# Kernel tuning notes

Hardware: AMD Instinct MI355X
Metric: run time of the kernel (lower is better)

Reference implementation:

```python
import jax, jax.numpy as jnp
import numpy as np
import math

N_NODES = 100000
D = 64
N_EDGES = 1280000
LN_EPS = 1e-5


def setup_inputs() -> dict:
    key = jax.random.key(0)
    ks = jax.random.split(key, 8)
    x = jax.random.normal(ks[0], (N_NODES, D), dtype=jnp.float32)
    edge_index = jax.random.randint(ks[1], (2, N_EDGES), 0, N_NODES, dtype=jnp.int64)
    # xavier_uniform with gain=0.1 for weight matrices
    limit = 0.1 * math.sqrt(6.0 / (D + D))
    qk_w = jax.random.uniform(ks[2], (D, D), dtype=jnp.float32, minval=-limit, maxval=limit)
    v_w = jax.random.uniform(ks[3], (D, D), dtype=jnp.float32, minval=-limit, maxval=limit)
    o_w = jax.random.uniform(ks[4], (D, D), dtype=jnp.float32, minval=-limit, maxval=limit)
    qk_b = jnp.zeros((D,), dtype=jnp.float32)
    v_b = jnp.zeros((D,), dtype=jnp.float32)
    o_b = jnp.zeros((D,), dtype=jnp.float32)
    ln_g = jnp.ones((D,), dtype=jnp.float32)
    ln_b = jnp.zeros((D,), dtype=jnp.float32)
    return {"x": x, "edge_index": edge_index, "qk_w": qk_w, "qk_b": qk_b,
            "v_w": v_w, "v_b": v_b, "o_w": o_w, "o_b": o_b,
            "ln_g": ln_g, "ln_b": ln_b}


def reference(x, edge_index, qk_w, qk_b, v_w, v_b, o_w, o_b, ln_g, ln_b):
    n = x.shape[0]
    # shared Q/K projection and V projection (torch Linear: x @ W^T + b)
    qk = x @ qk_w.T + qk_b            # [N, D]
    v = x @ v_w.T + v_b               # [N, D]

    src = edge_index[0]
    dst = edge_index[1]

    # edge-wise attention logits: <q[dst], k[src]> / sqrt(D), clamped
    scores = jnp.sum(qk[dst] * qk[src], axis=-1) / math.sqrt(v.shape[-1])  # [E]
    scores = jnp.clip(scores, -5.0, 5.0)

    # segment softmax over incoming edges of each destination node
    seg_max = jax.ops.segment_max(scores, dst, num_segments=n)   # [N], -inf for empty
    e = jnp.exp(scores - seg_max[dst])                           # [E]
    seg_sum = jax.ops.segment_sum(e, dst, num_segments=n)        # [N]
    attn = e / seg_sum[dst]                                      # [E]

    # weighted scatter-add aggregation (nodes with no in-edges stay zero)
    out = jax.ops.segment_sum(attn[:, None] * v[src], dst, num_segments=n)  # [N, D]

    out = out @ o_w.T + o_b

    # LayerNorm(out + residual)
    h = out + x
    mu = jnp.mean(h, axis=-1, keepdims=True)
    var = jnp.mean(jnp.square(h - mu), axis=-1, keepdims=True)
    h = (h - mu) * jax.lax.rsqrt(var + LN_EPS)
    return h * ln_g + ln_b
```

## Files before the change

### kernel.cpp

```cpp
#include <hip/hip_runtime.h>
#include <hip/hip_bf16.h>
#include <math.h>

#define DD 64
#define CAP 64
#define BINSZ 256
#define SLOTS 16
#define EPB 1024
#define NBINS 391
#define LN_EPS 1e-5f

typedef float v2f __attribute__((ext_vector_type(2)));
typedef __attribute__((ext_vector_type(8))) short bf16x8;
typedef __attribute__((ext_vector_type(4))) float f32x4;

__device__ __forceinline__ float bf2f(unsigned short u) {
    return __uint_as_float(((unsigned)u) << 16);
}
__device__ __forceinline__ short f2bf(float f) {
    __hip_bfloat16 h = __float2bfloat16(f);
    return *reinterpret_cast<short*>(&h);
}
__device__ __forceinline__ bf16x8 cvt8(const float* p) {
    float4 a = *(const float4*)p;
    float4 b = *(const float4*)(p + 4);
    bf16x8 r;
    r[0] = f2bf(a.x); r[1] = f2bf(a.y); r[2] = f2bf(a.z); r[3] = f2bf(a.w);
    r[4] = f2bf(b.x); r[5] = f2bf(b.y); r[6] = f2bf(b.z); r[7] = f2bf(b.w);
    return r;
}
__device__ __forceinline__ unsigned char f2fp8(float f) {
    return (unsigned char)(__builtin_amdgcn_cvt_pk_fp8_f32(f, 0.f, 0, false) & 0xff);
}

__global__ __launch_bounds__(256) void prep_kernel(
    const float* __restrict__ x,
    const float* __restrict__ qk_w, const float* __restrict__ qk_b,
    const float* __restrict__ v_w,  const float* __restrict__ v_b,
    const int* __restrict__ eidx, int* __restrict__ cnttab,
    unsigned* __restrict__ ebuf,
    __hip_bfloat16* __restrict__ qk, unsigned char* __restrict__ kv,
    int n, int E, int AB)
{
    __shared__ int lhist[NBINS];
    __shared__ unsigned char lkv[64 * 128];
    __shared__ unsigned short lq[64 * 64];

    int bid = blockIdx.x;
    int tid = threadIdx.x;
    if (bid < AB) {
        for (int b = tid; b < NBINS; b += 256) lhist[b] = 0;
        __syncthreads();
        int nv = E >> 2;
        int i4 = bid * 256 + tid;
        unsigned* slab = ebuf + (size_t)bid * NBINS * SLOTS;
        if (i4 < nv) {
            uint4 d = ((const uint4*)(eidx + E))[i4];
            uint4 s = ((const uint4*)(eidx))[i4];
            #pragma unroll
            for (int c = 0; c < 4; ++c) {
                unsigned dd = (c == 0) ? d.x : (c == 1) ? d.y
                            : (c == 2) ? d.z : d.w;
                unsigned ss = (c == 0) ? s.x : (c == 1) ? s.y
                            : (c == 2) ? s.z : s.w;
                int bin = dd >> 8;
                int r = atomicAdd(&lhist[bin], 1);
                if (r < SLOTS)
                    slab[bin * SLOTS + r] = (ss << 8) | (dd & 255);
            }
        }
        __syncthreads();
        int* mycnt = cnttab + bid * NBINS;
        for (int b = tid; b < NBINS; b += 256)
            mycnt[b] = min(lhist[b], SLOTS);
    } else {
        int pbid = bid - AB;
        int wave = tid >> 6, lane = tid & 63;
        int node0 = pbid * 64 + wave * 16;
        int lr = lane & 15;
        int lk = (lane >> 4) << 3;

        if (node0 < n) {
            int arow = min(node0 + lr, n - 1);
            const float* xr = x + (size_t)arow * 64 + lk;
            bf16x8 A0 = cvt8(xr);
            bf16x8 A1 = cvt8(xr + 32);

            float qbias[4] = {qk_b[lr], qk_b[16 + lr], qk_b[32 + lr], qk_b[48 + lr]};
            float vbias[4] = {v_b[lr],  v_b[16 + lr],  v_b[32 + lr],  v_b[48 + lr]};

            f32x4 z = {0.f, 0.f, 0.f, 0.f};
            f32x4 accq[4], accv[4];
            #pragma unroll
            for (int ct = 0; ct < 4; ++ct) {
                const float* wq = qk_w + (size_t)(ct * 16 + lr) * 64 + lk;
                bf16x8 Bq0 = cvt8(wq);
                bf16x8 Bq1 = cvt8(wq + 32);
                f32x4 aq = __builtin_amdgcn_mfma_f32_16x16x32_bf16(A0, Bq0, z, 0, 0, 0);
                aq = __builtin_amdgcn_mfma_f32_16x16x32_bf16(A1, Bq1, aq, 0, 0, 0);
                accq[ct] = aq;
                const float* wv = v_w + (size_t)(ct * 16 + lr) * 64 + lk;
                bf16x8 Bv0 = cvt8(wv);
                bf16x8 Bv1 = cvt8(wv + 32);
                f32x4 av = __builtin_amdgcn_mfma_f32_16x16x32_bf16(A0, Bv0, z, 0, 0, 0);
                av = __builtin_amdgcn_mfma_f32_16x16x32_bf16(A1, Bv1, av, 0, 0, 0);
                accv[ct] = av;
            }
            #pragma unroll
            for (int ct = 0; ct < 4; ++ct) {
                int dim  = ct * 16 + lr;
                int koff = ((dim >> 2) << 3) + (dim & 3);
                #pragma unroll
                for (int r = 0; r < 4; ++r) {
                    int ndl = wave * 16 + ((lane >> 4) << 2) + r;
                    float q = accq[ct][r] + qbias[ct];
                    float v = accv[ct][r] + vbias[ct];
                    lq[ndl * 64 + dim] = (unsigned short)f2bf(q);
                    lkv[ndl * 128 + koff]     = f2fp8(q);
                    lkv[ndl * 128 + koff + 4] = f2fp8(v);
                }
            }
        }
        __syncthreads();
        int row = tid >> 2;
        size_t gnode = (size_t)pbid * 64 + row;
        if (gnode < (size_t)n) {
            const uint4* skv = (const uint4*)(lkv + tid * 32);
            uint4* dkv = (uint4*)(kv + (size_t)pbid * 64 * 128 + tid * 32);
            dkv[0] = skv[0];
            dkv[1] = skv[1];
            const uint4* sq = (const uint4*)((const unsigned char*)lq + tid * 32);
            uint4* dq = (uint4*)((unsigned char*)qk + (size_t)pbid * 64 * 128 + tid * 32);
            dq[0] = sq[0];
            dq[1] = sq[1];
        }
    }
}

__global__ __launch_bounds__(512) void bucket_kernel(
    const int* __restrict__ cnttab, const unsigned* __restrict__ ebuf,
    int* __restrict__ deg, int* __restrict__ bucket, int n, int NPB)
{
    __shared__ int lbkt[BINSZ * CAP];
    __shared__ int ldeg[BINSZ];
    int bin = blockIdx.x, tid = threadIdx.x;
    if (tid < BINSZ) ldeg[tid] = 0;
    __syncthreads();
    for (int c = tid; c < NPB; c += 512) {
        int cnt = cnttab[c * NBINS + bin];
        const unsigned* run = ebuf + ((size_t)c * NBINS + bin) * SLOTS;
        for (int r = 0; r < cnt; ++r) {
            unsigned e = run[r];
            int rel = e & 255;
            int rr = atomicAdd(&ldeg[rel], 1);
            if (rr < CAP) lbkt[(rel << 6) + rr] = (int)(e >> 8);
        }
    }
    __syncthreads();
    size_t gbase = (size_t)(bin << 8) << 6;
    int node0 = bin << 8;
    const uint4* src = (const uint4*)lbkt;
    uint4* dst = (uint4*)(bucket + gbase);
    for (int i = tid; i < BINSZ * CAP / 4; i += 512) {
        if (node0 + (i >> 4) < n) dst[i] = src[i];
    }
    if (tid < BINSZ) {
        int node = node0 + tid;
        if (node < n) deg[node] = min(ldeg[tid], CAP);
    }
}

__global__ __launch_bounds__(256) void attn_kernel(
    const __hip_bfloat16* __restrict__ qk, const unsigned char* __restrict__ kv,
    const int* __restrict__ deg, const int* __restrict__ bucket,
    __hip_bfloat16* __restrict__ outd, int n)
{
    int tid = threadIdx.x;
    int wave = tid >> 6, lane = tid & 63;
    int node = blockIdx.x * 4 + wave;
    if (node >= n) return;

    int sub = lane >> 4;
    int sl  = lane & 15;

    ushort4 qu = *(const ushort4*)(qk + ((size_t)node << 6) + (sl << 2));
    v2f qlo = {bf2f(qu.x), bf2f(qu.y)};
    v2f qhi = {bf2f(qu.z), bf2f(qu.w)};
    int dn = deg[node];
    int medge = bucket[((size_t)node << 6) + lane];

    float s = 0.f;
    v2f acclo = {0.f, 0.f};
    v2f acchi = {0.f, 0.f};
    const float ESCALE = 0.18033688f;

    for (int base = 0; base < dn; base += 16) {
        int m1 = dn - 1;
        int i0 = base + sub;
        int i1 = i0 + 4, i2 = i0 + 8, i3 = i0 + 12;
        int s0 = __shfl(medge, min(i0, m1));
        int s1 = __shfl(medge, min(i1, m1));
        int s2 = __shfl(medge, min(i2, m1));
        int s3 = __shfl(medge, min(i3, m1));
        uint2 w0 = *(const uint2*)(kv + ((unsigned)s0 << 7) + (sl << 3));
        uint2 w1 = *(const uint2*)(kv + ((unsigned)s1 << 7) + (sl << 3));
        uint2 w2 = *(const uint2*)(kv + ((unsigned)s2 << 7) + (sl << 3));
        uint2 w3 = *(const uint2*)(kv + ((unsigned)s3 << 7) + (sl << 3));
        v2f t0 = qlo * __builtin_amdgcn_cvt_pk_f32_fp8(w0.x, false)
               + qhi * __builtin_amdgcn_cvt_pk_f32_fp8(w0.x, true);
        v2f t1 = qlo * __builtin_amdgcn_cvt_pk_f32_fp8(w1.x, false)
               + qhi * __builtin_amdgcn_cvt_pk_f32_fp8(w1.x, true);
        v2f t2 = qlo * __builtin_amdgcn_cvt_pk_f32_fp8(w2.x, false)
               + qhi * __builtin_amdgcn_cvt_pk_f32_fp8(w2.x, true);
        v2f t3 = qlo * __builtin_amdgcn_cvt_pk_f32_fp8(w3.x, false)
               + qhi * __builtin_amdgcn_cvt_pk_f32_fp8(w3.x, true);
        float p0 = t0.x + t0.y;
        float p1 = t1.x + t1.y;
        float p2 = t2.x + t2.y;
        float p3 = t3.x + t3.y;
        #pragma unroll
        for (int w = 1; w <= 8; w <<= 1) {
            p0 += __shfl_xor(p0, w); p1 += __shfl_xor(p1, w);
            p2 += __shfl_xor(p2, w); p3 += __shfl_xor(p3, w);
        }
        float pe0 = (i0 < dn) ? __builtin_amdgcn_exp2f(p0 * ESCALE) : 0.f;
        float pe1 = (i1 < dn) ? __builtin_amdgcn_exp2f(p1 * ESCALE) : 0.f;
        float pe2 = (i2 < dn) ? __builtin_amdgcn_exp2f(p2 * ESCALE) : 0.f;
        float pe3 = (i3 < dn) ? __builtin_amdgcn_exp2f(p3 * ESCALE) : 0.f;
        s += (pe0 + pe1) + (pe2 + pe3);
        acclo += __builtin_amdgcn_cvt_pk_f32_fp8(w0.y, false) * pe0;
        acchi += __builtin_amdgcn_cvt_pk_f32_fp8(w0.y, true)  * pe0;
        acclo += __builtin_amdgcn_cvt_pk_f32_fp8(w1.y, false) * pe1;
        acchi += __builtin_amdgcn_cvt_pk_f32_fp8(w1.y, true)  * pe1;
        acclo += __builtin_amdgcn_cvt_pk_f32_fp8(w2.y, false) * pe2;
        acchi += __builtin_amdgcn_cvt_pk_f32_fp8(w2.y, true)  * pe2;
        acclo += __builtin_amdgcn_cvt_pk_f32_fp8(w3.y, false) * pe3;
        acchi += __builtin_amdgcn_cvt_pk_f32_fp8(w3.y, true)  * pe3;
    }

    float a0 = acclo.x, a1 = acclo.y, a2 = acchi.x, a3 = acchi.y;
    s  += __shfl_xor(s, 16);  s  += __shfl_xor(s, 32);
    a0 += __shfl_xor(a0, 16); a0 += __shfl_xor(a0, 32);
    a1 += __shfl_xor(a1, 16); a1 += __shfl_xor(a1, 32);
    a2 += __shfl_xor(a2, 16); a2 += __shfl_xor(a2, 32);
    a3 += __shfl_xor(a3, 16); a3 += __shfl_xor(a3, 32);

    float inv = (dn > 0) ? (1.0f / s) : 0.f;
    if (sub == 0) {
        ushort4 o;
        o.x = (unsigned short)f2bf(a0 * inv);
        o.y = (unsigned short)f2bf(a1 * inv);
        o.z = (unsigned short)f2bf(a2 * inv);
        o.w = (unsigned short)f2bf(a3 * inv);
        *(ushort4*)(outd + ((size_t)node << 6) + (sl << 2)) = o;
    }
}

__global__ __launch_bounds__(256) void epi_kernel(
    const __hip_bfloat16* __restrict__ outd, const float* __restrict__ x,
    const float* __restrict__ o_w, const float* __restrict__ o_b,
    const float* __restrict__ ln_g, const float* __restrict__ ln_b,
    float* __restrict__ out, int n)
{
    int tid = threadIdx.x;
    int wave = tid >> 6, lane = tid & 63;
    int node0 = blockIdx.x * 64 + wave * 16;
    if (node0 >= n) return;

    int lr = lane & 15;
    int lk = (lane >> 4) << 3;

    int arow = min(node0 + lr, n - 1);
    const __hip_bfloat16* odr = outd + (size_t)arow * 64 + lk;
    bf16x8 A0 = *(const bf16x8*)odr;
    bf16x8 A1 = *(const bf16x8*)(odr + 32);

    f32x4 z = {0.f, 0.f, 0.f, 0.f};
    f32x4 acc[4];
    #pragma unroll
    for (int ct = 0; ct < 4; ++ct) {
        const float* wo = o_w + (size_t)(ct * 16 + lr) * 64 + lk;
        bf16x8 B0 = cvt8(wo);
        bf16x8 B1 = cvt8(wo + 32);
        f32x4 a = __builtin_amdgcn_mfma_f32_16x16x32_bf16(A0, B0, z, 0, 0, 0);
        a = __builtin_amdgcn_mfma_f32_16x16x32_bf16(A1, B1, a, 0, 0, 0);
        acc[ct] = a;
    }
    float ob[4] = {o_b[lr], o_b[16 + lr], o_b[32 + lr], o_b[48 + lr]};
    float lg[4] = {ln_g[lr], ln_g[16 + lr], ln_g[32 + lr], ln_g[48 + lr]};
    float lb[4] = {ln_b[lr], ln_b[16 + lr], ln_b[32 + lr], ln_b[48 + lr]};

    #pragma unroll
    for (int r = 0; r < 4; ++r) {
        int nd = node0 + ((lane >> 4) << 2) + r;
        if (nd >= n) break;
        float h[4];
        #pragma unroll
        for (int ct = 0; ct < 4; ++ct)
            h[ct] = acc[ct][r] + ob[ct] + x[(size_t)nd * 64 + ct * 16 + lr];
        float m = (h[0] + h[1]) + (h[2] + h[3]);
        #pragma unroll
        for (int w = 1; w <= 8; w <<= 1) m += __shfl_xor(m, w);
        m *= (1.f / 64.f);
        float d0 = h[0] - m, d1 = h[1] - m, d2 = h[2] - m, d3 = h[3] - m;
        float vv = (d0 * d0 + d1 * d1) + (d2 * d2 + d3 * d3);
        #pragma unroll
        for (int w = 1; w <= 8; w <<= 1) vv += __shfl_xor(vv, w);
        vv *= (1.f / 64.f);
        float rs = rsqrtf(vv + LN_EPS);
        float* op = out + (size_t)nd * 64 + lr;
        op[0]  = d0 * rs * lg[0] + lb[0];
        op[16] = d1 * rs * lg[1] + lb[1];
        op[32] = d2 * rs * lg[2] + lb[2];
        op[48] = d3 * rs * lg[3] + lb[3];
    }
}

extern "C" void kernel_launch(void* const* d_in, const int* in_sizes, int n_in,
                              void* d_out, int out_size, void* d_ws, size_t ws_size,
                              hipStream_t stream)
{
    const float* x    = (const float*)d_in[0];
    const int*   eidx = (const int*)  d_in[1];
    const float* qk_w = (const float*)d_in[2];
    const float* qk_b = (const float*)d_in[3];
    const float* v_w  = (const float*)d_in[4];
    const float* v_b  = (const float*)d_in[5];
    const float* o_w  = (const float*)d_in[6];
    const float* o_b  = (const float*)d_in[7];
    const float* ln_g = (const float*)d_in[8];
    const float* ln_b = (const float*)d_in[9];

    const int n = in_sizes[0] / DD;
    const int E = in_sizes[1] / 2;
    const int AB = (E + EPB - 1) / EPB;
    const int PB = (n + 63) / 64;

    char* ws = (char*)d_ws;
    size_t off = 0;
    __hip_bfloat16* qk = (__hip_bfloat16*)(ws + off); off += (size_t)n * 64 * 2;
    unsigned char* kv  = (unsigned char*)(ws + off); off += (size_t)n * 128;
    int* deg    = (int*)(ws + off); off += (size_t)n * 4;
    int* bucket = (int*)(ws + off); off += (size_t)n * CAP * 4;
    int* cnttab = (int*)(ws + off); off += (size_t)AB * NBINS * 4;
    unsigned* ebuf = (unsigned*)(ws + off); off += (size_t)AB * NBINS * SLOTS * 4;
    __hip_bfloat16* outd = (__hip_bfloat16*)(ws + off); off += (size_t)n * 64 * 2;

    prep_kernel<<<AB + PB, 256, 0, stream>>>(x, qk_w, qk_b, v_w, v_b,
                                             eidx, cnttab, ebuf, qk, kv, n, E, AB);
    bucket_kernel<<<NBINS, 512, 0, stream>>>(cnttab, ebuf, deg, bucket, n, AB);
    attn_kernel<<<(n + 3) / 4, 256, 0, stream>>>(qk, kv, deg, bucket, outd, n);
    epi_kernel<<<(n + 63) / 64, 256, 0, stream>>>(outd, x, o_w, o_b, ln_g, ln_b,
                                                  (float*)d_out, n);
}
```

Before: 127.8 us.

## Compact edge partition buffer via block-local counting sort with offsets

Replaces the fixed-slot per-bin slab layout with a block-local counting sort: each partition block computes bin histograms, prefix-scans them in shared memory, stages edges contiguously and writes a dense run plus (count, offset) pairs. Edges per block double and shared memory is unioned between the partition and projection paths. This shrinks the intermediate buffer and makes writes and the bucket kernel's reads contiguous, at the cost of a multi-step shared-memory scan with extra barriers. It also removes the per-bin slot cap, so no edges are truncated.

```diff
diff --git a/kernel.cpp b/kernel.cpp
--- a/kernel.cpp
+++ b/kernel.cpp
@@ -5,8 +5,7 @@
 #define DD 64
 #define CAP 64
 #define BINSZ 256
-#define SLOTS 16
-#define EPB 1024
+#define EPB 2048
 #define NBINS 391
 #define LN_EPS 1e-5f
 
@@ -33,46 +32,78 @@
     return (unsigned char)(__builtin_amdgcn_cvt_pk_fp8_f32(f, 0.f, 0, false) & 0xff);
 }
 
+struct PartSh { int lhist[512]; int lsa[512]; int lsb[512]; unsigned lstage[EPB]; };
+struct ProjSh { unsigned char lkv[64 * 128]; unsigned short lq[64 * 64]; };
+
 __global__ __launch_bounds__(256) void prep_kernel(
     const float* __restrict__ x,
     const float* __restrict__ qk_w, const float* __restrict__ qk_b,
     const float* __restrict__ v_w,  const float* __restrict__ v_b,
-    const int* __restrict__ eidx, int* __restrict__ cnttab,
+    const int* __restrict__ eidx, int2* __restrict__ cotab,
     unsigned* __restrict__ ebuf,
     __hip_bfloat16* __restrict__ qk, unsigned char* __restrict__ kv,
     int n, int E, int AB)
 {
-    __shared__ int lhist[NBINS];
-    __shared__ unsigned char lkv[64 * 128];
-    __shared__ unsigned short lq[64 * 64];
+    __shared__ union { PartSh p; ProjSh j; } sh;
 
     int bid = blockIdx.x;
     int tid = threadIdx.x;
     if (bid < AB) {
-        for (int b = tid; b < NBINS; b += 256) lhist[b] = 0;
+        for (int b = tid; b < 512; b += 256) sh.p.lhist[b] = 0;
         __syncthreads();
         int nv = E >> 2;
-        int i4 = bid * 256 + tid;
-        unsigned* slab = ebuf + (size_t)bid * NBINS * SLOTS;
-        if (i4 < nv) {
-            uint4 d = ((const uint4*)(eidx + E))[i4];
-            uint4 s = ((const uint4*)(eidx))[i4];
-            #pragma unroll
-            for (int c = 0; c < 4; ++c) {
-                unsigned dd = (c == 0) ? d.x : (c == 1) ? d.y
-                            : (c == 2) ? d.z : d.w;
-                unsigned ss = (c == 0) ? s.x : (c == 1) ? s.y
-                            : (c == 2) ? s.z : s.w;
-                int bin = dd >> 8;
-                int r = atomicAdd(&lhist[bin], 1);
-                if (r < SLOTS)
-                    slab[bin * SLOTS + r] = (ss << 8) | (dd & 255);
+        const uint4* dst4 = (const uint4*)(eidx + E);
+        const uint4* src4 = (const uint4*)(eidx);
+        uint4 d[2], s[2];
+        int rnk[8];
+        bool ok[2];
+        #pragma unroll
+        for (int g = 0; g < 2; ++g) {
+            int i4 = bid * 512 + tid + g * 256;
+            ok[g] = i4 < nv;
+            if (ok[g]) {
+                d[g] = dst4[i4];
+                s[g] = src4[i4];
+                #pragma unroll
+                for (int c = 0; c < 4; ++c) {
+                    unsigned dd = (c == 0) ? d[g].x : (c == 1) ? d[g].y
+                                : (c == 2) ? d[g].z : d[g].w;
+                    rnk[g * 4 + c] = atomicAdd(&sh.p.lhist[dd >> 8], 1);
+                }
             }
         }
         __syncthreads();
-        int* mycnt = cnttab + bid * NBINS;
+        for (int e = tid; e < 512; e += 256) sh.p.lsa[e] = sh.p.lhist[e];
+        __syncthreads();
+        int* cur = sh.p.lsa;
+        int* nxt = sh.p.lsb;
+        for (int st = 1; st < 512; st <<= 1) {
+            for (int e = tid; e < 512; e += 256)
+                nxt[e] = cur[e] + ((e >= st) ? cur[e - st] : 0);
+            __syncthreads();
+            int* t = cur; cur = nxt; nxt = t;
+        }
+        #pragma unroll
+        for (int g = 0; g < 2; ++g) {
+            if (ok[g]) {
+                #pragma unroll
+                for (int c = 0; c < 4; ++c) {
+                    unsigned dd = (c == 0) ? d[g].x : (c == 1) ? d[g].y
+                                : (c == 2) ? d[g].z : d[g].w;
+                    unsigned ss = (c == 0) ? s[g].x : (c == 1) ? s[g].y
+                                : (c == 2) ? s[g].z : s[g].w;
+                    int bin = dd >> 8;
+                    int off = bin ? cur[bin - 1] : 0;
+                    sh.p.lstage[off + rnk[g * 4 + c]] = (ss << 8) | (dd & 255);
+                }
+            }
+        }
+        __syncthreads();
+        unsigned* myebuf = ebuf + (size_t)bid * EPB;
+        for (int e = tid; e < EPB; e += 256) myebuf[e] = sh.p.lstage[e];
+        int2* myco = cotab + (size_t)bid * NBINS;
         for (int b = tid; b < NBINS; b += 256)
-            mycnt[b] = min(lhist[b], SLOTS);
+            myco[b] = make_int2(sh.p.lhist[b], b ? cur[b - 1] : 0);
     } else {
         int pbid = bid - AB;
         int wave = tid >> 6, lane = tid & 63;
@@ -115,9 +146,9 @@
                     int ndl = wave * 16 + ((lane >> 4) << 2) + r;
                     float q = accq[ct][r] + qbias[ct];
                     float v = accv[ct][r] + vbias[ct];
-                    lq[ndl * 64 + dim] = (unsigned short)f2bf(q);
-                    lkv[ndl * 128 + koff]     = f2fp8(q);
-                    lkv[ndl * 128 + koff + 4] = f2fp8(v);
+                    sh.j.lq[ndl * 64 + dim] = (unsigned short)f2bf(q);
+                    sh.j.lkv[ndl * 128 + koff]     = f2fp8(q);
+                    sh.j.lkv[ndl * 128 + koff + 4] = f2fp8(v);
                 }
             }
         }
@@ -125,11 +156,11 @@
         int row = tid >> 2;
         size_t gnode = (size_t)pbid * 64 + row;
         if (gnode < (size_t)n) {
-            const uint4* skv = (const uint4*)(lkv + tid * 32);
+            const uint4* skv = (const uint4*)(sh.j.lkv + tid * 32);
             uint4* dkv = (uint4*)(kv + (size_t)pbid * 64 * 128 + tid * 32);
             dkv[0] = skv[0];
             dkv[1] = skv[1];
-            const uint4* sq = (const uint4*)((const unsigned char*)lq + tid * 32);
+            const uint4* sq = (const uint4*)((const unsigned char*)sh.j.lq + tid * 32);
             uint4* dq = (uint4*)((unsigned char*)qk + (size_t)pbid * 64 * 128 + tid * 32);
             dq[0] = sq[0];
             dq[1] = sq[1];
@@ -138,7 +169,7 @@
 }
 
 __global__ __launch_bounds__(512) void bucket_kernel(
-    const int* __restrict__ cnttab, const unsigned* __restrict__ ebuf,
+    const int2* __restrict__ cotab, const unsigned* __restrict__ ebuf,
     int* __restrict__ deg, int* __restrict__ bucket, int n, int NPB)
 {
     __shared__ int lbkt[BINSZ * CAP];
@@ -147,9 +178,9 @@
     if (tid < BINSZ) ldeg[tid] = 0;
     __syncthreads();
     for (int c = tid; c < NPB; c += 512) {
-        int cnt = cnttab[c * NBINS + bin];
-        const unsigned* run = ebuf + ((size_t)c * NBINS + bin) * SLOTS;
-        for (int r = 0; r < cnt; ++r) {
+        int2 co = cotab[(size_t)c * NBINS + bin];
+        const unsigned* run = ebuf + (size_t)c * EPB + co.y;
+        for (int r = 0; r < co.x; ++r) {
             unsigned e = run[r];
             int rel = e & 255;
             int rr = atomicAdd(&ldeg[rel], 1);
@@ -342,13 +373,13 @@
     unsigned char* kv  = (unsigned char*)(ws + off); off += (size_t)n * 128;
     int* deg    = (int*)(ws + off); off += (size_t)n * 4;
     int* bucket = (int*)(ws + off); off += (size_t)n * CAP * 4;
-    int* cnttab = (int*)(ws + off); off += (size_t)AB * NBINS * 4;
-    unsigned* ebuf = (unsigned*)(ws + off); off += (size_t)AB * NBINS * SLOTS * 4;
+    int2* cotab = (int2*)(ws + off); off += (size_t)AB * NBINS * 8;
+    unsigned* ebuf = (unsigned*)(ws + off); off += (size_t)AB * EPB * 4;
     __hip_bfloat16* outd = (__hip_bfloat16*)(ws + off); off += (size_t)n * 64 * 2;
 
     prep_kernel<<<AB + PB, 256, 0, stream>>>(x, qk_w, qk_b, v_w, v_b,
-                                             eidx, cnttab, ebuf, qk, kv, n, E, AB);
-    bucket_kernel<<<NBINS, 512, 0, stream>>>(cnttab, ebuf, deg, bucket, n, AB);
+                                             eidx, cotab, ebuf, qk, kv, n, E, AB);
+    bucket_kernel<<<NBINS, 512, 0, stream>>>(cotab, ebuf, deg, bucket, n, AB);
     attn_kernel<<<(n + 3) / 4, 256, 0, stream>>>(qk, kv, deg, bucket, outd, n);
     epi_kernel<<<(n + 63) / 64, 256, 0, stream>>>(outd, x, o_w, o_b, ln_g, ln_b,
                                                   (float*)d_out, n);
```

Measured after the change: 121.0 us. 1.06x faster.
